# Performance work log

Hardware: AMD Instinct MI355X
Metric: run time of the kernel (lower is better)

## Reference

```python
import jax, jax.numpy as jnp
import numpy as np

B, N, D = 512, 100000, 64
TAU = 1e-4            # gumbel-softmax temperature from source
SIM_RATIO = 0.5       # similarity_ratio init kwarg
COS_EPS = 1e-6


def setup_inputs() -> dict:
    key = jax.random.key(0)
    k1, k2, k3, k4, k5 = jax.random.split(key, 5)
    need_replace = jax.random.randint(k1, (B, 2), 0, N, dtype=jnp.int64) if jax.config.jax_enable_x64 else jax.random.randint(k1, (B, 2), 0, N, dtype=jnp.int32)
    union_feature = jax.random.normal(k2, (B, 2 * D), dtype=jnp.float32)
    all_items = jax.random.normal(k3, (N, D), dtype=jnp.float32) * 0.1
    W = jax.random.normal(k4, (D, 2 * D), dtype=jnp.float32) * 0.05
    b = jax.random.normal(k5, (D,), dtype=jnp.float32) * 0.01
    return {"need_replace": need_replace, "union_feature": union_feature,
            "all_items": all_items, "W": W, "b": b}


def _cosine(a, b):
    # torch.nn.CosineSimilarity(dim=1, eps=1e-6): dot / max(||a||*||b||, eps)
    dot = jnp.sum(a * b, axis=1)
    na = jnp.linalg.norm(a, axis=1)
    nb = jnp.linalg.norm(b, axis=1)
    return dot / jnp.maximum(na * nb, COS_EPS)


def reference(need_replace, union_feature, all_items, W, b):
    item_ids = need_replace[:, 1]
    items_emb = all_items[item_ids]                      # [B, D]
    uif = union_feature @ W.T + b                        # [B, D] (nn.Linear)
    score = uif @ all_items.T                            # [B, N]

    # gumbel_softmax(tau=1e-4, hard=True), training branch
    g = jax.random.gumbel(jax.random.key(42), score.shape, dtype=score.dtype)
    y_soft = jax.nn.softmax((score + g) / TAU, axis=-1)  # [B, N]
    idx = jnp.argmax(y_soft, axis=-1)                    # [B]
    y_hard = jax.nn.one_hot(idx, N, dtype=score.dtype)
    P = y_hard + y_soft - jax.lax.stop_gradient(y_soft)  # straight-through hard one-hot

    item_sequence = jnp.arange(N, dtype=score.dtype)[None, :]
    replaceable_items = jnp.sum(P * item_sequence, axis=-1).astype(jnp.int32)
    replaceable_feat = P @ all_items                     # [B, D]

    sim = _cosine(items_emb, replaceable_feat)
    sim = (sim + 1.0) / 2.0                              # regularize_similarity
    labels = jnp.full((B,), SIM_RATIO, dtype=sim.dtype)
    similarity_loss = jnp.mean((sim - labels) ** 2)      # SimilarityMarginLoss (assumed MSE-to-margin)
    return replaceable_items, replaceable_feat, similarity_loss, jnp.mean(sim)
```

## Files before the change

kernel.cpp:

```cpp
#include <hip/hip_runtime.h>
#include <cstdint>

#define NITEMS   100000
#define BROWS    512
#define DDIM     64
#define S_BLOCKS 391
#define IPB      256
#define FB_X     64
#define FB_Y     8
#define FB_CHUNK 1568
#define OUT_FEAT 512
#define OUT_LOSS (512 + 512 * 64)
#define OUT_MSIM (OUT_LOSS + 1)

#define BITS_RAW_T 4284334592u
#define G_TE       6.001f

typedef __attribute__((ext_vector_type(8)))  short  bf16x8;
typedef __attribute__((ext_vector_type(16))) float  f32x16;
typedef unsigned long long u64;
typedef uint32_t u32;

#define ROTL(x, r) __builtin_amdgcn_alignbit((x), (x), 32u - (r))

__device__ __forceinline__ u32 threefry_0_42_xor(u32 e) {
    const u32 K1 = 42u;
    const u32 K2 = 0x1BD11BDAu ^ 42u;
    u32 x0 = 0u;
    u32 x1 = e + K1;
#define TFR(r) { x0 += x1; x1 = ROTL(x1, r) ^ x0; }
    TFR(13u) TFR(15u) TFR(26u) TFR(6u)
    x0 += K1;  x1 += K2 + 1u;
    TFR(17u) TFR(29u) TFR(16u) TFR(24u)
    x0 += K2;  x1 += 2u;
    TFR(13u) TFR(15u) TFR(26u) TFR(6u)
    x1 += K1 + 3u;
    TFR(17u) TFR(29u) TFR(16u) TFR(24u)
    x0 += K1;  x1 += K2 + 4u;
    TFR(13u) TFR(15u) TFR(26u) TFR(6u)
    x0 += K2;  x1 += 5u;
#undef TFR
    return x0 ^ x1;
}

__device__ __forceinline__ void threefry_pair(u32 ea, u32 eb, u32& oa, u32& ob) {
    const u32 K1 = 42u;
    const u32 K2 = 0x1BD11BDAu ^ 42u;
    u32 a0 = 0u, a1 = ea + K1;
    u32 b0 = 0u, b1 = eb + K1;
#define TFR2(r) { a0 += a1; b0 += b1; a1 = ROTL(a1, r) ^ a0; b1 = ROTL(b1, r) ^ b0; }
    TFR2(13u) TFR2(15u) TFR2(26u) TFR2(6u)
    a0 += K1; a1 += K2 + 1u;  b0 += K1; b1 += K2 + 1u;
    TFR2(17u) TFR2(29u) TFR2(16u) TFR2(24u)
    a0 += K2; a1 += 2u;       b0 += K2; b1 += 2u;
    TFR2(13u) TFR2(15u) TFR2(26u) TFR2(6u)
    a1 += K1 + 3u;            b1 += K1 + 3u;
    TFR2(17u) TFR2(29u) TFR2(16u) TFR2(24u)
    a0 += K1; a1 += K2 + 4u;  b0 += K1; b1 += K2 + 4u;
    TFR2(13u) TFR2(15u) TFR2(26u) TFR2(6u)
    a0 += K2; a1 += 5u;       b0 += K2; b1 += 5u;
#undef TFR2
    oa = a0 ^ a1; ob = b0 ^ b1;
}

__device__ __forceinline__ float gumbel_from_bits(u32 b) {
    float f = __uint_as_float((b >> 9) | 0x3F800000u) - 1.0f;
    f = fmaxf(f, 1.17549435e-38f);
    return -logf(-logf(f));
}
__device__ __forceinline__ u32 order_map(float v) {
    u32 x = __float_as_uint(v);
    return (x & 0x80000000u) ? ~x : (x | 0x80000000u);
}
__device__ __forceinline__ float unpack_val(u64 p) {
    u32 x = (u32)(p >> 32);
    u32 f = (x & 0x80000000u) ? (x & 0x7FFFFFFFu) : ~x;
    return __uint_as_float(f);
}
__device__ __forceinline__ short f32_to_bf16_rne(float f) {
    u32 b = __float_as_uint(f);
    u32 r = (b + 0x7FFFu + ((b >> 16) & 1u)) >> 16;
    return (short)r;
}
__device__ __forceinline__ float bf16_to_f32(short h) {
    return __uint_as_float(((u32)(uint16_t)h) << 16);
}

__global__ void prep_kernel(const float* __restrict__ UF, const float* __restrict__ W,
                            const float* __restrict__ bias, const float* __restrict__ A,
                            float* __restrict__ uif, float* __restrict__ unorm,
                            float* __restrict__ wsAM4, int* __restrict__ cnt,
                            int* __restrict__ done, float* __restrict__ out) {
    const int t = threadIdx.x, b = blockIdx.x;
    if (b == 0) {
        if (t == 0) { *cnt = 0; out[OUT_LOSS] = 0.f; out[OUT_MSIM] = 0.f; }
        done[t] = 0; done[t + 256] = 0;
    }
    if (b < 128) {
        __shared__ float Wt[128 * 65];
        for (int i = t; i < 8192; i += 256) {
            int d = i >> 7, k = i & 127;
            Wt[k * 65 + d] = W[i];
        }
        __syncthreads();
        const int row = b * 4 + (t >> 6);
        const int d   = t & 63;
        const float* u = UF + row * 128;
        float s = 0.f;
#pragma unroll 4
        for (int k = 0; k < 128; k++) s = fmaf(u[k], Wt[k * 65 + d], s);
        s += bias[d];
        uif[row * 64 + d] = s;
        float q = s * s;
#pragma unroll
        for (int o = 32; o >= 1; o >>= 1) q += __shfl_xor(q, o);
        if (d == 0) unorm[row] = sqrtf(q);
    } else {
        const int item = (b - 128) * 256 + t;
        float q = 0.f;
        if (item < NITEMS) {
            const float4* r = (const float4*)(A + (size_t)item * DDIM);
#pragma unroll
            for (int k = 0; k < 16; k++) {
                float4 x = r[k];
                q = fmaf(x.x, x.x, q); q = fmaf(x.y, x.y, q);
                q = fmaf(x.z, x.z, q); q = fmaf(x.w, x.w, q);
            }
        }
        float n = sqrtf(q);
#pragma unroll
        for (int o = 32; o >= 1; o >>= 1) n = fmaxf(n, __shfl_xor(n, o));
        if ((t & 63) == 0) wsAM4[(b - 128) * 4 + (t >> 6)] = n;
    }
}

__global__ __launch_bounds__(256, 6) void phase1_kernel(
        const float* __restrict__ A, const float* __restrict__ uif,
        u64* __restrict__ wsT1, float* __restrict__ wsB) {
    __shared__ bf16x8 sh_ah[4 * 64];
    __shared__ bf16x8 sh_al[4 * 64];
    const int tid  = threadIdx.x;
    const int lane = tid & 63;
    const int wv   = tid >> 6;
    const int rg   = blockIdx.y;
    const int sb   = blockIdx.x;
    const int itembase = sb * IPB;
    const int ntiles = min(8, (NITEMS - itembase + 31) >> 5);
    const int row   = rg * 128 + wv * 32 + (lane & 31);
    const int khalf = (lane >> 5) * 8;

    bf16x8 uh[4], ul[4];
#pragma unroll
    for (int s = 0; s < 4; s++) {
        const float* src = uif + row * 64 + khalf + 16 * s;
        float4 v0 = *(const float4*)src;
        float4 v1 = *(const float4*)(src + 4);
        float vv[8] = {v0.x, v0.y, v0.z, v0.w, v1.x, v1.y, v1.z, v1.w};
        bf16x8 h, l2;
#pragma unroll
        for (int j = 0; j < 8; j++) {
            short hh = f32_to_bf16_rne(vv[j]);
            float r  = vv[j] - bf16_to_f32(hh);
            h[j] = hh; l2[j] = f32_to_bf16_rne(r);
        }
        uh[s] = h; ul[s] = l2;
    }

    u64 t1p = 0ull; float t1f = -3.0e38f, t2f = -3.0e38f, sm = -3.0e38f;
    const u32 rowbase_e = (u32)row * (u32)NITEMS;

    const int s_i   = tid & 31;
    const int s_c   = tid >> 5;
    const int s_dst = (s_c >> 1) * 64 + s_i + 32 * (s_c & 1);
    const float* s_srcbase = A + (size_t)s_i * 64 + 8 * s_c;

    float4 p0 = *(const float4*)(s_srcbase + (size_t)itembase * 64);
    float4 p1 = *(const float4*)(s_srcbase + (size_t)itembase * 64 + 4);

    for (int t = 0; t < ntiles; t++) {
        const int tb = itembase + t * 32;
        bf16x8 h, l2;
        {
            float vv[8] = {p0.x, p0.y, p0.z, p0.w, p1.x, p1.y, p1.z, p1.w};
#pragma unroll
            for (int j = 0; j < 8; j++) {
                short hh = f32_to_bf16_rne(vv[j]);
                float r  = vv[j] - bf16_to_f32(hh);
                h[j] = hh; l2[j] = f32_to_bf16_rne(r);
            }
        }
        __syncthreads();
        sh_ah[s_dst] = h; sh_al[s_dst] = l2;
        __syncthreads();
        if (t + 1 < ntiles) {
            const float* src = s_srcbase + (size_t)(tb + 32) * 64;
            p0 = *(const float4*)src;
            p1 = *(const float4*)(src + 4);
        }

        f32x16 acc;
#pragma unroll
        for (int z = 0; z < 16; z++) acc[z] = 0.0f;
#pragma unroll
        for (int s = 0; s < 4; s++) {
            bf16x8 ah = sh_ah[s * 64 + lane];
            bf16x8 al = sh_al[s * 64 + lane];
            acc = __builtin_amdgcn_mfma_f32_32x32x16_bf16(ah, uh[s], acc, 0, 0, 0);
            acc = __builtin_amdgcn_mfma_f32_32x32x16_bf16(al, uh[s], acc, 0, 0, 0);
            acc = __builtin_amdgcn_mfma_f32_32x32x16_bf16(ah, ul[s], acc, 0, 0, 0);
        }

        const int ib4 = tb + 4 * (lane >> 5);
#pragma unroll
        for (int i = 0; i < 16; i += 2) {
            const int il0 = (i & 3) + 8 * (i >> 2);
            const int il1 = ((i + 1) & 3) + 8 * ((i + 1) >> 2);
            const int item0 = ib4 + il0;
            const int item1 = ib4 + il1;
            u32 r0, r1;
            threefry_pair(rowbase_e + (u32)item0, rowbase_e + (u32)item1, r0, r1);
            float sA = acc[i], sB = acc[i + 1];
            sm = fmaxf(sm, fmaxf(sA, sB));
            if (r0 >= BITS_RAW_T) {
                float v = sA + gumbel_from_bits(r0);
                if (v > t1f) {
                    t2f = t1f; t1f = v;
                    t1p = ((u64)order_map(v) << 32) | (u32)(~(u32)item0);
                } else t2f = fmaxf(t2f, v);
            }
            if (r1 >= BITS_RAW_T) {
                float v = sB + gumbel_from_bits(r1);
                if (v > t1f) {
                    t2f = t1f; t1f = v;
                    t1p = ((u64)order_map(v) << 32) | (u32)(~(u32)item1);
                } else t2f = fmaxf(t2f, v);
            }
        }
    }

    float bnd = fmaxf(t2f, sm + G_TE);
    {
        u64   op = __shfl_xor(t1p, 32);
        float of = __shfl_xor(t1f, 32);
        float ob = __shfl_xor(bnd, 32);
        if (op > t1p) { bnd = fmaxf(fmaxf(bnd, ob), t1f); t1p = op; t1f = of; }
        else          { bnd = fmaxf(fmaxf(bnd, ob), of); }
    }
    if (lane < 32) {
        wsT1[(size_t)row * S_BLOCKS + sb] = t1p;
        wsB [(size_t)row * S_BLOCKS + sb] = bnd;
    }
}

__global__ void merge_kernel(const u64* __restrict__ wsT1, const float* __restrict__ wsB,
                             const float* __restrict__ wsAM4, const float* __restrict__ unorm,
                             const float* __restrict__ A, const int* __restrict__ need_replace,
                             u64* __restrict__ packed, int* __restrict__ rowlist,
                             int* __restrict__ cnt, float* __restrict__ out) {
    const int row = blockIdx.x, t = threadIdx.x;
    float am = 0.f;
    for (int i = t; i < S_BLOCKS * 4; i += 64) am = fmaxf(am, wsAM4[i]);
    u64 p1 = 0ull; float f1 = -3.0e38f, f2 = -3.0e38f;
    for (int sbk = t; sbk < S_BLOCKS; sbk += 64) {
        u64   ep = wsT1[(size_t)row * S_BLOCKS + sbk];
        float e2 = wsB [(size_t)row * S_BLOCKS + sbk];
        if (ep > p1) { f2 = fmaxf(fmaxf(f1, e2), f2); p1 = ep; f1 = unpack_val(ep); }
        else         { float v = unpack_val(ep); f2 = fmaxf(f2, fmaxf(v, e2)); }
    }
#pragma unroll
    for (int off = 1; off < 64; off <<= 1) {
        u64   op  = __shfl_xor(p1, off);
        float of1 = __shfl_xor(f1, off);
        float of2 = __shfl_xor(f2, off);
        am = fmaxf(am, __shfl_xor(am, off));
        if (op > p1) { f2 = fmaxf(fmaxf(f1, of2), f2); p1 = op; f1 = of1; }
        else         { f2 = fmaxf(f2, fmaxf(of1, of2)); }
    }
    const float E = 1.5e-4f * unorm[row] * am + 3.0e-5f;
    if (f1 - f2 > 2.0f * E) {
        const int idx = (int)(~(u32)(p1 & 0xFFFFFFFFull));
        float fr = A[(size_t)idx * DDIM + t];
        out[OUT_FEAT + row * DDIM + t] = fr;
        int   item = need_replace[2 * row + 1];
        float fa   = A[(size_t)item * DDIM + t];
        float dot = fa * fr, na2 = fa * fa, nb2 = fr * fr;
#pragma unroll
        for (int o = 32; o >= 1; o >>= 1) {
            dot += __shfl_down(dot, o);
            na2 += __shfl_down(na2, o);
            nb2 += __shfl_down(nb2, o);
        }
        if (t == 0) {
            out[row] = (float)idx;
            float denom = fmaxf(sqrtf(na2) * sqrtf(nb2), 1e-6f);
            float sim = (dot / denom + 1.0f) * 0.5f;
            float d = sim - 0.5f;
            atomicAdd(&out[OUT_LOSS], d * d * (1.0f / 512.0f));
            atomicAdd(&out[OUT_MSIM], sim * (1.0f / 512.0f));
        }
    } else if (t == 0) {
        packed[row] = 0ull;
        rowlist[atomicAdd(cnt, 1)] = row;
    }
}

__global__ void fallback_kernel(const float* __restrict__ A, const float* __restrict__ uif,
                                const int* __restrict__ rowlist, const int* __restrict__ cnt,
                                const int* __restrict__ need_replace,
                                u64* __restrict__ packed, int* __restrict__ done,
                                float* __restrict__ out) {
    __shared__ float Us[64];
    __shared__ int   sh_last;
    const int t  = threadIdx.x;
    const int xb = blockIdx.x;
    const int total = *cnt;
    const int iend = min((xb + 1) * FB_CHUNK, NITEMS);

    for (int li = blockIdx.y; li < total; li += FB_Y) {
        const int row = rowlist[li];
        __syncthreads();
        if (t < 64) Us[t] = uif[row * 64 + t];
        __syncthreads();
        u64 pk = 0ull;
        for (int item = xb * FB_CHUNK + t; item < iend; item += 256) {
            u32 rb  = threefry_0_42_xor((u32)row * (u32)NITEMS + (u32)item);
            float g = gumbel_from_bits(rb);
            const float4* a4 = (const float4*)(A + (size_t)item * DDIM);
            float s0 = 0.f, s1 = 0.f;
#pragma unroll
            for (int k = 0; k < 16; k += 2) {
                float4 x = a4[k];
                float4 y = a4[k + 1];
                s0 = fmaf(x.x, Us[4*k    ], s0);
                s0 = fmaf(x.y, Us[4*k + 1], s0);
                s0 = fmaf(x.z, Us[4*k + 2], s0);
                s0 = fmaf(x.w, Us[4*k + 3], s0);
                s1 = fmaf(y.x, Us[4*k + 4], s1);
                s1 = fmaf(y.y, Us[4*k + 5], s1);
                s1 = fmaf(y.z, Us[4*k + 6], s1);
                s1 = fmaf(y.w, Us[4*k + 7], s1);
            }
            float v = (s0 + s1) + g;
            u64 c = ((u64)order_map(v) << 32) | (u32)(~(u32)item);
            pk = (c > pk) ? c : pk;
        }
#pragma unroll
        for (int off = 1; off < 64; off <<= 1) {
            u64 o = __shfl_xor(pk, off);
            pk = (o > pk) ? o : pk;
        }
        if ((t & 63) == 0) atomicMax(&packed[row], pk);
        __syncthreads();
        if (t == 0) {
            __threadfence();
            sh_last = (atomicAdd(&done[li], 1) == FB_X - 1) ? 1 : 0;
        }
        __syncthreads();
        if (sh_last && t < 64) {
            u64 fin = atomicMax(&packed[row], 0ull);
            const int idx = (int)(~(u32)(fin & 0xFFFFFFFFull));
            float fr = A[(size_t)idx * DDIM + t];
            out[OUT_FEAT + row * DDIM + t] = fr;
            int   item = need_replace[2 * row + 1];
            float fa   = A[(size_t)item * DDIM + t];
            float dot = fa * fr, na2 = fa * fa, nb2 = fr * fr;
#pragma unroll
            for (int o = 32; o >= 1; o >>= 1) {
                dot += __shfl_down(dot, o);
                na2 += __shfl_down(na2, o);
                nb2 += __shfl_down(nb2, o);
            }
            if (t == 0) {
                out[row] = (float)idx;
                float denom = fmaxf(sqrtf(na2) * sqrtf(nb2), 1e-6f);
                float sim = (dot / denom + 1.0f) * 0.5f;
                float d = sim - 0.5f;
                atomicAdd(&out[OUT_LOSS], d * d * (1.0f / 512.0f));
                atomicAdd(&out[OUT_MSIM], sim * (1.0f / 512.0f));
            }
        }
        __syncthreads();
    }
}

extern "C" void kernel_launch(void* const* d_in, const int* in_sizes, int n_in,
                              void* d_out, int out_size, void* d_ws, size_t ws_size,
                              hipStream_t stream) {
    (void)in_sizes; (void)n_in; (void)out_size; (void)ws_size;
    const int*   need_replace = (const int*)d_in[0];
    const float* UF           = (const float*)d_in[1];
    const float* A            = (const float*)d_in[2];
    const float* W            = (const float*)d_in[3];
    const float* bias         = (const float*)d_in[4];
    float* out = (float*)d_out;

    char* ws = (char*)d_ws;
    u64*   wsT1    = (u64*)  (ws);
    float* wsB     = (float*)(ws + 1601536);
    float* uif     = (float*)(ws + 2402304);
    u64*   packed  = (u64*)  (ws + 2533376);
    float* unorm   = (float*)(ws + 2537472);
    float* wsAM4   = (float*)(ws + 2539520);
    int*   rowlist = (int*)  (ws + 2545776);
    int*   cnt     = (int*)  (ws + 2547824);
    int*   done    = (int*)  (ws + 2547828);

    prep_kernel<<<519, 256, 0, stream>>>(UF, W, bias, A, uif, unorm, wsAM4, cnt, done, out);
    phase1_kernel<<<dim3(S_BLOCKS, 4), 256, 0, stream>>>(A, uif, wsT1, wsB);
    merge_kernel<<<BROWS, 64, 0, stream>>>(wsT1, wsB, wsAM4, unorm, A, need_replace,
                                           packed, rowlist, cnt, out);
    fallback_kernel<<<dim3(FB_X, FB_Y), 256, 0, stream>>>(A, uif, rowlist, cnt,
                                                          need_replace, packed, done, out);
}
```

Baseline: 256.6 us.

## Stride phase1 tiles over a fixed 256-wide grid and batch threefry four-wide

The phase1 grid drops from 391×4 blocks, each owning a contiguous 256-item chunk, to 256×4 blocks that walk 32-item tiles with a stride of 256. The total block count then lines up with the machine and avoids a small trailing wave of leftover blocks. Each block now handles more tiles, and the merge kernel reads fewer per-row partial results. The threefry hash is also computed for four items at a time instead of two, adding instruction-level parallelism at the cost of higher register pressure.

```diff
diff --git a/kernel.cpp b/kernel.cpp
--- a/kernel.cpp
+++ b/kernel.cpp
@@ -5,7 +5,9 @@
 #define BROWS    512
 #define DDIM     64
 #define S_BLOCKS 391
-#define IPB      256
+#define AM4_N    (S_BLOCKS * 4)
+#define SB_OUT   256
+#define NTILES   3125
 #define FB_X     64
 #define FB_Y     8
 #define FB_CHUNK 1568
@@ -43,24 +45,34 @@
     return x0 ^ x1;
 }
 
-__device__ __forceinline__ void threefry_pair(u32 ea, u32 eb, u32& oa, u32& ob) {
+__device__ __forceinline__ void threefry_quad(u32 e0, u32 e1, u32 e2, u32 e3,
+                                              u32& r0, u32& r1, u32& r2, u32& r3) {
     const u32 K1 = 42u;
     const u32 K2 = 0x1BD11BDAu ^ 42u;
-    u32 a0 = 0u, a1 = ea + K1;
-    u32 b0 = 0u, b1 = eb + K1;
-#define TFR2(r) { a0 += a1; b0 += b1; a1 = ROTL(a1, r) ^ a0; b1 = ROTL(b1, r) ^ b0; }
-    TFR2(13u) TFR2(15u) TFR2(26u) TFR2(6u)
+    u32 a0 = 0u, a1 = e0 + K1;
+    u32 b0 = 0u, b1 = e1 + K1;
+    u32 c0 = 0u, c1 = e2 + K1;
+    u32 d0 = 0u, d1 = e3 + K1;
+#define TFR4(r) { a0 += a1; b0 += b1; c0 += c1; d0 += d1; \
+                  a1 = ROTL(a1, r) ^ a0; b1 = ROTL(b1, r) ^ b0; \
+                  c1 = ROTL(c1, r) ^ c0; d1 = ROTL(d1, r) ^ d0; }
+    TFR4(13u) TFR4(15u) TFR4(26u) TFR4(6u)
     a0 += K1; a1 += K2 + 1u;  b0 += K1; b1 += K2 + 1u;
-    TFR2(17u) TFR2(29u) TFR2(16u) TFR2(24u)
+    c0 += K1; c1 += K2 + 1u;  d0 += K1; d1 += K2 + 1u;
+    TFR4(17u) TFR4(29u) TFR4(16u) TFR4(24u)
     a0 += K2; a1 += 2u;       b0 += K2; b1 += 2u;
-    TFR2(13u) TFR2(15u) TFR2(26u) TFR2(6u)
+    c0 += K2; c1 += 2u;       d0 += K2; d1 += 2u;
+    TFR4(13u) TFR4(15u) TFR4(26u) TFR4(6u)
     a1 += K1 + 3u;            b1 += K1 + 3u;
-    TFR2(17u) TFR2(29u) TFR2(16u) TFR2(24u)
+    c1 += K1 + 3u;            d1 += K1 + 3u;
+    TFR4(17u) TFR4(29u) TFR4(16u) TFR4(24u)
     a0 += K1; a1 += K2 + 4u;  b0 += K1; b1 += K2 + 4u;
-    TFR2(13u) TFR2(15u) TFR2(26u) TFR2(6u)
+    c0 += K1; c1 += K2 + 4u;  d0 += K1; d1 += K2 + 4u;
+    TFR4(13u) TFR4(15u) TFR4(26u) TFR4(6u)
     a0 += K2; a1 += 5u;       b0 += K2; b1 += 5u;
-#undef TFR2
-    oa = a0 ^ a1; ob = b0 ^ b1;
+    c0 += K2; c1 += 5u;       d0 += K2; d1 += 5u;
+#undef TFR4
+    r0 = a0 ^ a1; r1 = b0 ^ b1; r2 = c0 ^ c1; r3 = d0 ^ d1;
 }
 
 __device__ __forceinline__ float gumbel_from_bits(u32 b) {
@@ -143,9 +155,7 @@
     const int lane = tid & 63;
     const int wv   = tid >> 6;
     const int rg   = blockIdx.y;
-    const int sb   = blockIdx.x;
-    const int itembase = sb * IPB;
-    const int ntiles = min(8, (NITEMS - itembase + 31) >> 5);
+    const int xb   = blockIdx.x;
     const int row   = rg * 128 + wv * 32 + (lane & 31);
     const int khalf = (lane >> 5) * 8;
 
@@ -174,11 +184,12 @@
     const int s_dst = (s_c >> 1) * 64 + s_i + 32 * (s_c & 1);
     const float* s_srcbase = A + (size_t)s_i * 64 + 8 * s_c;
 
-    float4 p0 = *(const float4*)(s_srcbase + (size_t)itembase * 64);
-    float4 p1 = *(const float4*)(s_srcbase + (size_t)itembase * 64 + 4);
-
-    for (int t = 0; t < ntiles; t++) {
-        const int tb = itembase + t * 32;
+    int t_idx = xb;
+    float4 p0 = *(const float4*)(s_srcbase + (size_t)t_idx * (32 * 64));
+    float4 p1 = *(const float4*)(s_srcbase + (size_t)t_idx * (32 * 64) + 4);
+
+    while (t_idx < NTILES) {
+        const int tb = t_idx * 32;
         bf16x8 h, l2;
         {
             float vv[8] = {p0.x, p0.y, p0.z, p0.w, p1.x, p1.y, p1.z, p1.w};
@@ -192,8 +203,9 @@
         __syncthreads();
         sh_ah[s_dst] = h; sh_al[s_dst] = l2;
         __syncthreads();
-        if (t + 1 < ntiles) {
-            const float* src = s_srcbase + (size_t)(tb + 32) * 64;
+        t_idx += SB_OUT;
+        if (t_idx < NTILES) {
+            const float* src = s_srcbase + (size_t)t_idx * (32 * 64);
             p0 = *(const float4*)src;
             p1 = *(const float4*)(src + 4);
         }
@@ -212,27 +224,40 @@
 
         const int ib4 = tb + 4 * (lane >> 5);
 #pragma unroll
-        for (int i = 0; i < 16; i += 2) {
-            const int il0 = (i & 3) + 8 * (i >> 2);
-            const int il1 = ((i + 1) & 3) + 8 * ((i + 1) >> 2);
-            const int item0 = ib4 + il0;
-            const int item1 = ib4 + il1;
-            u32 r0, r1;
-            threefry_pair(rowbase_e + (u32)item0, rowbase_e + (u32)item1, r0, r1);
-            float sA = acc[i], sB = acc[i + 1];
-            sm = fmaxf(sm, fmaxf(sA, sB));
+        for (int i = 0; i < 16; i += 4) {
+            const int i0 = ib4 + 2 * i;
+            u32 r0, r1, r2, r3;
+            threefry_quad(rowbase_e + (u32)(i0 + 0), rowbase_e + (u32)(i0 + 1),
+                          rowbase_e + (u32)(i0 + 2), rowbase_e + (u32)(i0 + 3),
+                          r0, r1, r2, r3);
+            float sA = acc[i], sB = acc[i + 1], sC = acc[i + 2], sD = acc[i + 3];
+            sm = fmaxf(sm, fmaxf(fmaxf(sA, sB), fmaxf(sC, sD)));
             if (r0 >= BITS_RAW_T) {
                 float v = sA + gumbel_from_bits(r0);
                 if (v > t1f) {
                     t2f = t1f; t1f = v;
-                    t1p = ((u64)order_map(v) << 32) | (u32)(~(u32)item0);
+                    t1p = ((u64)order_map(v) << 32) | (u32)(~(u32)(i0 + 0));
                 } else t2f = fmaxf(t2f, v);
             }
             if (r1 >= BITS_RAW_T) {
                 float v = sB + gumbel_from_bits(r1);
                 if (v > t1f) {
                     t2f = t1f; t1f = v;
-                    t1p = ((u64)order_map(v) << 32) | (u32)(~(u32)item1);
+                    t1p = ((u64)order_map(v) << 32) | (u32)(~(u32)(i0 + 1));
+                } else t2f = fmaxf(t2f, v);
+            }
+            if (r2 >= BITS_RAW_T) {
+                float v = sC + gumbel_from_bits(r2);
+                if (v > t1f) {
+                    t2f = t1f; t1f = v;
+                    t1p = ((u64)order_map(v) << 32) | (u32)(~(u32)(i0 + 2));
+                } else t2f = fmaxf(t2f, v);
+            }
+            if (r3 >= BITS_RAW_T) {
+                float v = sD + gumbel_from_bits(r3);
+                if (v > t1f) {
+                    t2f = t1f; t1f = v;
+                    t1p = ((u64)order_map(v) << 32) | (u32)(~(u32)(i0 + 3));
                 } else t2f = fmaxf(t2f, v);
             }
         }
@@ -247,8 +272,8 @@
         else          { bnd = fmaxf(fmaxf(bnd, ob), of); }
     }
     if (lane < 32) {
-        wsT1[(size_t)row * S_BLOCKS + sb] = t1p;
-        wsB [(size_t)row * S_BLOCKS + sb] = bnd;
+        wsT1[(size_t)row * SB_OUT + xb] = t1p;
+        wsB [(size_t)row * SB_OUT + xb] = bnd;
     }
 }
 
@@ -259,11 +284,11 @@
                              int* __restrict__ cnt, float* __restrict__ out) {
     const int row = blockIdx.x, t = threadIdx.x;
     float am = 0.f;
-    for (int i = t; i < S_BLOCKS * 4; i += 64) am = fmaxf(am, wsAM4[i]);
+    for (int i = t; i < AM4_N; i += 64) am = fmaxf(am, wsAM4[i]);
     u64 p1 = 0ull; float f1 = -3.0e38f, f2 = -3.0e38f;
-    for (int sbk = t; sbk < S_BLOCKS; sbk += 64) {
-        u64   ep = wsT1[(size_t)row * S_BLOCKS + sbk];
-        float e2 = wsB [(size_t)row * S_BLOCKS + sbk];
+    for (int sbk = t; sbk < SB_OUT; sbk += 64) {
+        u64   ep = wsT1[(size_t)row * SB_OUT + sbk];
+        float e2 = wsB [(size_t)row * SB_OUT + sbk];
         if (ep > p1) { f2 = fmaxf(fmaxf(f1, e2), f2); p1 = ep; f1 = unpack_val(ep); }
         else         { float v = unpack_val(ep); f2 = fmaxf(f2, fmaxf(v, e2)); }
     }
@@ -396,17 +421,17 @@
 
     char* ws = (char*)d_ws;
     u64*   wsT1    = (u64*)  (ws);
-    float* wsB     = (float*)(ws + 1601536);
-    float* uif     = (float*)(ws + 2402304);
-    u64*   packed  = (u64*)  (ws + 2533376);
-    float* unorm   = (float*)(ws + 2537472);
-    float* wsAM4   = (float*)(ws + 2539520);
-    int*   rowlist = (int*)  (ws + 2545776);
-    int*   cnt     = (int*)  (ws + 2547824);
-    int*   done    = (int*)  (ws + 2547828);
+    float* wsB     = (float*)(ws + 1048576);
+    float* uif     = (float*)(ws + 1572864);
+    u64*   packed  = (u64*)  (ws + 1703936);
+    float* unorm   = (float*)(ws + 1708032);
+    float* wsAM4   = (float*)(ws + 1710080);
+    int*   rowlist = (int*)  (ws + 1716336);
+    int*   cnt     = (int*)  (ws + 1718384);
+    int*   done    = (int*)  (ws + 1718388);
 
     prep_kernel<<<519, 256, 0, stream>>>(UF, W, bias, A, uif, unorm, wsAM4, cnt, done, out);
-    phase1_kernel<<<dim3(S_BLOCKS, 4), 256, 0, stream>>>(A, uif, wsT1, wsB);
+    phase1_kernel<<<dim3(SB_OUT, 4), 256, 0, stream>>>(A, uif, wsT1, wsB);
     merge_kernel<<<BROWS, 64, 0, stream>>>(wsT1, wsB, wsAM4, unorm, A, need_replace,
                                            packed, rowlist, cnt, out);
     fallback_kernel<<<dim3(FB_X, FB_Y), 256, 0, stream>>>(A, uif, rowlist, cnt,
```

New measurement: 251.3 us. 1.02x faster.
